# Kernel tuning notes

Hardware: AMD Instinct MI355X
Metric: run time of the kernel (lower is better)

The kernel has to match this reference:

```python
import jax, jax.numpy as jnp
from jax import lax
import numpy as np

B, C, Hf, Wf = 4, 256, 64, 64
COMP = max(C // 4, 16)  # 64
SCALE, K_UP, K_ENC = 2, 5, 3
EPS = 1e-5


def setup_inputs() -> dict:
    key = jax.random.key(0)
    ks = jax.random.split(key, 6)
    x = jax.random.normal(ks[0], (B, C, Hf, Wf), dtype=jnp.float32)
    w_comp = jax.random.normal(ks[1], (COMP, C), dtype=jnp.float32) * (1.0 / np.sqrt(C))
    bn_gamma = jnp.ones((COMP,), dtype=jnp.float32)
    bn_beta = jnp.zeros((COMP,), dtype=jnp.float32)
    bn_mean = jax.random.normal(ks[2], (COMP,), dtype=jnp.float32) * 0.1
    bn_var = jax.random.uniform(ks[3], (COMP,), dtype=jnp.float32, minval=0.5, maxval=1.5)
    w_enc = jax.random.normal(ks[4], (K_UP * K_UP * SCALE * SCALE, COMP, K_ENC, K_ENC), dtype=jnp.float32) * (1.0 / np.sqrt(COMP * K_ENC * K_ENC))
    return {"x": x, "w_comp": w_comp, "bn_gamma": bn_gamma, "bn_beta": bn_beta,
            "bn_mean": bn_mean, "bn_var": bn_var, "w_enc": w_enc}


def reference(x, w_comp, bn_gamma, bn_beta, bn_mean, bn_var, w_enc):
    b, c, h, w = x.shape
    s, k = SCALE, K_UP
    # 1x1 compression conv
    comp = jnp.einsum('bchw,oc->bohw', x, w_comp)
    # BatchNorm (eval-style, running stats) + SiLU
    inv = (bn_gamma / jnp.sqrt(bn_var + EPS))[:, None, None]
    bn = (comp - bn_mean[:, None, None]) * inv + bn_beta[:, None, None]
    act = bn * jax.nn.sigmoid(bn)
    # encoder conv -> per-pixel reassembly kernels, channels = k^2 * s^2 (k2 outer, s2 inner)
    mask = lax.conv_general_dilated(act, w_enc, (1, 1), ((1, 1), (1, 1)),
                                    dimension_numbers=('NCHW', 'OIHW', 'NCHW'))
    mask = mask.reshape(b, k * k, s * s, h, w)
    mask = jax.nn.softmax(mask, axis=1)  # softmax over k_up*k_up window
    # unfold: gather 5x5 neighborhoods (pad 2), k = dy*5+dx row-major like F.unfold
    pad = k // 2
    xp = jnp.pad(x, ((0, 0), (0, 0), (pad, pad), (pad, pad)))
    patches = jnp.stack([xp[:, :, dy:dy + h, dx:dx + w]
                         for dy in range(k) for dx in range(k)], axis=2)  # (b,c,k2,h,w)
    # content-aware weighted sum per sub-pixel position
    out = jnp.einsum('bksij,bckij->bcsij', mask, patches)  # (b,c,s2,h,w)
    # s2 -> (s0,s1); pixel (i*s+s0, j*s+s1)
    out = out.reshape(b, c, s, s, h, w).transpose(0, 1, 4, 2, 5, 3).reshape(b, c, h * s, w * s)
    return out
```

## Files before the change

### kernel.cpp

```cpp
#include <hip/hip_runtime.h>
#include <hip/hip_bf16.h>
#include <hip/hip_fp16.h>
#include <math.h>

#define B_ 4
#define C_ 256
#define H_ 64
#define W_ 64
#define COMP_ 64
#define K2_ 25
#define HW_ (H_*W_)
#define EPS_ 1e-5f
#define WTE_STRIDE 26

typedef float v2f __attribute__((ext_vector_type(2)));
#define FMA2(a, b, c) __builtin_elementwise_fma((a), (b), (c))

__global__ void k_transpose(const float* __restrict__ w_comp,
                            const float* __restrict__ w_enc,
                            float* __restrict__ wTc,
                            float* __restrict__ wTe) {
    int t = blockIdx.x * 256 + threadIdx.x;
    if (t < COMP_ * C_) {
        int o = t & 63;
        int c = t >> 6;
        wTc[t] = w_comp[o * C_ + c];
    } else {
        int t2 = t - COMP_ * C_;
        if (t2 < 100 * COMP_ * 9) {
            int k2 = t2 % 25;
            int r = t2 / 25;
            int s2 = r & 3; r >>= 2;
            int q = r % 9;
            int o = r / 9;
            wTe[((o * 9 + q) * 4 + s2) * WTE_STRIDE + k2] =
                w_enc[(((k2 * 4 + s2) * COMP_) + o) * 9 + q];
        }
    }
}

__global__ void __launch_bounds__(1024)
k_compress(const float* __restrict__ x, const float* __restrict__ wTc,
           const float* __restrict__ gamma, const float* __restrict__ beta,
           const float* __restrict__ mean, const float* __restrict__ var,
           float* __restrict__ act) {
    __shared__ v2f red[32 * 64];
    const int tx = threadIdx.x;
    const int ty = threadIdx.y;
    const int tz = threadIdx.z;
    const int ogu = __builtin_amdgcn_readfirstlane(ty);
    const int cgu = __builtin_amdgcn_readfirstlane(tz);
    const int b = blockIdx.y;
    const int p0 = blockIdx.x * 64;

    v2f acc2[4];
#pragma unroll
    for (int k = 0; k < 4; ++k) acc2[k] = (v2f){0.f, 0.f};

    const float* xb = x + (size_t)b * C_ * HW_ + p0 + tx;
#pragma unroll 8
    for (int cl = 0; cl < 128; ++cl) {
        int c = cgu * 128 + cl;
        float xv = xb[c * HW_];
        const v2f* w2 = (const v2f*)(wTc + c * COMP_ + ogu * 8);
        v2f xv2 = (v2f){xv, xv};
#pragma unroll
        for (int k = 0; k < 4; ++k)
            acc2[k] = FMA2(xv2, w2[k], acc2[k]);
    }

    if (tz == 1) {
#pragma unroll
        for (int k = 0; k < 4; ++k) red[(ty * 4 + k) * 64 + tx] = acc2[k];
    }
    __syncthreads();
    if (tz == 0) {
#pragma unroll
        for (int k = 0; k < 4; ++k) {
            v2f s = acc2[k] + red[(ty * 4 + k) * 64 + tx];
            int o0 = ty * 8 + 2 * k;
#pragma unroll
            for (int h = 0; h < 2; ++h) {
                int o = o0 + h;
                float sv = (h == 0) ? s.x : s.y;
                float iv = gamma[o] * rsqrtf(var[o] + EPS_);
                float bn = (sv - mean[o]) * iv + beta[o];
                float sg = 1.f / (1.f + __expf(-bn));
                act[((b * COMP_ + o) * HW_) + p0 + tx] = bn * sg;
            }
        }
    }
}

__global__ void __launch_bounds__(1024)
k_encoder(const float* __restrict__ act, const float* __restrict__ wTe,
          __half* __restrict__ maskT) {
    __shared__ float sact[13312];
    const int tx = threadIdx.x;
    const int ty = threadIdx.y;
    const int tz = threadIdx.z;
    const int tid = (tz * 4 + ty) * 64 + tx;
    const int i = blockIdx.x;
    const int b = blockIdx.y;
    const int s2u = __builtin_amdgcn_readfirstlane(ty);
    const int ogu = __builtin_amdgcn_readfirstlane(tz);

    const float* ab = act + (size_t)b * COMP_ * HW_;
    for (int t = tid; t < 3 * COMP_ * 66; t += 1024) {
        int col = t % 66;
        int r = t / 66;
        int o = r & 63;
        int row = r >> 6;
        int gi = i + row - 1;
        int gj = col - 1;
        float v = 0.f;
        if ((unsigned)gi < 64u && (unsigned)gj < 64u)
            v = ab[(o * H_ + gi) * W_ + gj];
        sact[t] = v;
    }
    __syncthreads();

    v2f acc2[13];
#pragma unroll
    for (int k = 0; k < 13; ++k) acc2[k] = (v2f){0.f, 0.f};

#pragma unroll 2
    for (int oi = 0; oi < 16; ++oi) {
        int o = ogu * 16 + oi;
#pragma unroll
        for (int q = 0; q < 9; ++q) {
            const int dy = q / 3, dx = q % 3;
            float a = sact[(dy * COMP_ + o) * 66 + tx + dx];
            const float* wb = wTe + ((o * 9 + q) * 4 + s2u) * WTE_STRIDE;
            const v2f* w2 = (const v2f*)wb;
            v2f a2 = (v2f){a, a};
#pragma unroll
            for (int k = 0; k < 12; ++k)
                acc2[k] = FMA2(a2, w2[k], acc2[k]);
            acc2[12].x = fmaf(wb[24], a, acc2[12].x);
        }
    }
    __syncthreads();

    v2f* bufA = (v2f*)sact;
    v2f* bufB = bufA + 3328;
    const int rix = ty * 64 + tx;
    if (tz == 1) {
#pragma unroll
        for (int k = 0; k < 13; ++k) bufA[k * 256 + rix] = acc2[k];
    } else if (tz == 2) {
#pragma unroll
        for (int k = 0; k < 13; ++k) bufB[k * 256 + rix] = acc2[k];
    }
    __syncthreads();
    if (tz == 0) {
#pragma unroll
        for (int k = 0; k < 13; ++k) acc2[k] += bufA[k * 256 + rix];
    } else if (tz == 3) {
#pragma unroll
        for (int k = 0; k < 13; ++k) acc2[k] += bufB[k * 256 + rix];
    }
    __syncthreads();
    if (tz == 3) {
#pragma unroll
        for (int k = 0; k < 13; ++k) bufA[k * 256 + rix] = acc2[k];
    }
    __syncthreads();
    float ex[K2_];
    if (tz == 0) {
#pragma unroll
        for (int k = 0; k < 13; ++k) acc2[k] += bufA[k * 256 + rix];

        float mx = acc2[12].x;
#pragma unroll
        for (int k = 0; k < 12; ++k) mx = fmaxf(mx, fmaxf(acc2[k].x, acc2[k].y));
        float sum = 0.f;
#pragma unroll
        for (int k = 0; k < 12; ++k) {
            ex[2 * k]     = __expf(acc2[k].x - mx);
            ex[2 * k + 1] = __expf(acc2[k].y - mx);
            sum += ex[2 * k] + ex[2 * k + 1];
        }
        ex[24] = __expf(acc2[12].x - mx);
        sum += ex[24];
        float rs = 1.f / sum;
#pragma unroll
        for (int k = 0; k < K2_; ++k) ex[k] *= rs;
    }
    __syncthreads();

    __half* st = (__half*)sact;
    if (tz == 0) {
#pragma unroll
        for (int k = 0; k < K2_; ++k)
            st[tx * 100 + k * 4 + ty] = __float2half(ex[k]);
    }
    __syncthreads();

    float4* dst = (float4*)(maskT + ((size_t)b * HW_ + i * 64) * 100);
    const float4* src = (const float4*)st;
    if (tid < 800) dst[tid] = src[tid];
}

__global__ void __launch_bounds__(256)
k_reassemble(const float* __restrict__ x, const __half* __restrict__ maskT,
             float* __restrict__ out) {
    __shared__ __align__(16) __half smask[64 * 100];
    __shared__ __align__(16) float sx[5 * 68 * 20];
    const int tx = threadIdx.x;
    const int ty = threadIdx.y;
    const int tid = ty * 64 + tx;
    const int i = blockIdx.x;
    const int cc = blockIdx.y;
    const int b = blockIdx.z;

    {
        const float4* src = (const float4*)(maskT + ((size_t)b * HW_ + i * 64) * 100);
        float4* dst = (float4*)smask;
#pragma unroll
        for (int t = 0; t < 4; ++t) {
            int e = tid + t * 256;
            if (e < 800) dst[e] = src[e];
        }
    }

    const float* xb = x + ((size_t)b * C_ + cc * 16 + ty * 4) * HW_;
#pragma unroll
    for (int r = 0; r < 5; ++r) {
        const int gi = i + r - 2;
        const bool rowok = ((unsigned)gi < 64u);
        {
            float4 v = {0.f, 0.f, 0.f, 0.f};
            int gj = tx - 2;
            if (rowok && gj >= 0) {
                const float* p = xb + gi * W_ + gj;
                v.x = p[0];
                v.y = p[HW_];
                v.z = p[2 * HW_];
                v.w = p[3 * HW_];
            }
            *(float4*)&sx[(r * 68 + tx) * 20 + ty * 4] = v;
        }
        if (tid < 16) {
            int q = tid >> 2;
            int col = 64 + (tid & 3);
            int gj = col - 2;
            float4 v = {0.f, 0.f, 0.f, 0.f};
            if (rowok && gj < 64) {
                const float* p = x + ((size_t)b * C_ + cc * 16 + q * 4) * HW_ + gi * W_ + gj;
                v.x = p[0];
                v.y = p[HW_];
                v.z = p[2 * HW_];
                v.w = p[3 * HW_];
            }
            *(float4*)&sx[(r * 68 + col) * 20 + q * 4] = v;
        }
    }
    __syncthreads();

    v2f a01[4], a23[4];
#pragma unroll
    for (int cl = 0; cl < 4; ++cl) { a01[cl] = (v2f){0.f, 0.f}; a23[cl] = (v2f){0.f, 0.f}; }

    float4 xq = *(const float4*)&sx[(0 * 68 + tx + 0) * 20 + ty * 4];
    __half2 h01 = *(const __half2*)&smask[tx * 100 + 0];
    __half2 h23 = *(const __half2*)&smask[tx * 100 + 2];

#pragma unroll
    for (int k2 = 0; k2 < K2_; ++k2) {
        float4 xq_c = xq;
        __half2 h01_c = h01, h23_c = h23;
        if (k2 < K2_ - 1) {
            const int kn = k2 + 1;
            const int dy = kn / 5, dx = kn % 5;
            xq  = *(const float4*)&sx[(dy * 68 + tx + dx) * 20 + ty * 4];
            h01 = *(const __half2*)&smask[tx * 100 + kn * 4];
            h23 = *(const __half2*)&smask[tx * 100 + kn * 4 + 2];
        }
        float2 f01 = __half22float2(h01_c);
        float2 f23 = __half22float2(h23_c);
        v2f m01 = (v2f){f01.x, f01.y};
        v2f m23 = (v2f){f23.x, f23.y};
        float xc[4] = {xq_c.x, xq_c.y, xq_c.z, xq_c.w};
#pragma unroll
        for (int cl = 0; cl < 4; ++cl) {
            v2f xv2 = (v2f){xc[cl], xc[cl]};
            a01[cl] = FMA2(xv2, m01, a01[cl]);
            a23[cl] = FMA2(xv2, m23, a23[cl]);
        }
    }

#pragma unroll
    for (int cl = 0; cl < 4; ++cl) {
        int c = cc * 16 + ty * 4 + cl;
        float* op = out + (((size_t)(b * C_ + c) * 128 + 2 * i) * 128) + 2 * tx;
        *(float2*)op         = float2{a01[cl].x, a01[cl].y};
        *(float2*)(op + 128) = float2{a23[cl].x, a23[cl].y};
    }
}

extern "C" void kernel_launch(void* const* d_in, const int* in_sizes, int n_in,
                              void* d_out, int out_size, void* d_ws, size_t ws_size,
                              hipStream_t stream) {
    const float* x       = (const float*)d_in[0];
    const float* w_comp  = (const float*)d_in[1];
    const float* bn_g    = (const float*)d_in[2];
    const float* bn_b    = (const float*)d_in[3];
    const float* bn_m    = (const float*)d_in[4];
    const float* bn_v    = (const float*)d_in[5];
    const float* w_enc   = (const float*)d_in[6];
    float* out = (float*)d_out;

    float* ws    = (float*)d_ws;
    float* wTc   = ws;
    float* wTe   = ws + 16384;
    float* act   = ws + 16384 + 59904;
    __half* maskT = (__half*)(act + (size_t)B_ * COMP_ * HW_);

    k_transpose<<<289, 256, 0, stream>>>(w_comp, w_enc, wTc, wTe);
    k_compress<<<dim3(64, B_), dim3(64, 8, 2), 0, stream>>>(x, wTc, bn_g, bn_b, bn_m, bn_v, act);
    k_encoder<<<dim3(64, B_), dim3(64, 4, 4), 0, stream>>>(act, wTe, maskT);
    k_reassemble<<<dim3(64, 16, B_), dim3(64, 4), 0, stream>>>(x, maskT, out);
}
```

Baseline: 169.0 us.

## Stage compress input via LDS float4 loads, swizzle reassemble blocks, batch global loads

k_compress now loads its 256x64 x tile into LDS with float4 loads using 512 threads, and drops the two-way channel split and its reduction step. k_reassemble flattens its grid to 1D and applies an XCD-aware block swizzle so neighbouring rows share L2. It also issues all mask and x halo loads into registers before writing them to LDS, which exposes more memory-level parallelism. The trade-offs are fewer threads in the compress kernel, higher register pressure in reassemble, and a 68KB LDS footprint for compress that limits occupancy.

```diff
diff --git a/kernel.cpp b/kernel.cpp
--- a/kernel.cpp
+++ b/kernel.cpp
@@ -39,29 +39,37 @@
     }
 }
 
-__global__ void __launch_bounds__(1024)
+__global__ void __launch_bounds__(512)
 k_compress(const float* __restrict__ x, const float* __restrict__ wTc,
            const float* __restrict__ gamma, const float* __restrict__ beta,
            const float* __restrict__ mean, const float* __restrict__ var,
            float* __restrict__ act) {
-    __shared__ v2f red[32 * 64];
+    __shared__ float sx[256 * 68];
     const int tx = threadIdx.x;
     const int ty = threadIdx.y;
-    const int tz = threadIdx.z;
+    const int tid = ty * 64 + tx;
     const int ogu = __builtin_amdgcn_readfirstlane(ty);
-    const int cgu = __builtin_amdgcn_readfirstlane(tz);
     const int b = blockIdx.y;
     const int p0 = blockIdx.x * 64;
 
+    const float* xb = x + (size_t)b * C_ * HW_ + p0;
+#pragma unroll
+    for (int l = 0; l < 8; ++l) {
+        int e = tid + l * 512;
+        int c = e >> 4;
+        int p4 = (e & 15) << 2;
+        float4 v4 = *(const float4*)(xb + (size_t)c * HW_ + p4);
+        *(float4*)&sx[c * 68 + p4] = v4;
+    }
+    __syncthreads();
+
     v2f acc2[4];
 #pragma unroll
     for (int k = 0; k < 4; ++k) acc2[k] = (v2f){0.f, 0.f};
 
-    const float* xb = x + (size_t)b * C_ * HW_ + p0 + tx;
 #pragma unroll 8
-    for (int cl = 0; cl < 128; ++cl) {
-        int c = cgu * 128 + cl;
-        float xv = xb[c * HW_];
+    for (int c = 0; c < 256; ++c) {
+        float xv = sx[c * 68 + tx];
         const v2f* w2 = (const v2f*)(wTc + c * COMP_ + ogu * 8);
         v2f xv2 = (v2f){xv, xv};
 #pragma unroll
@@ -69,25 +77,17 @@
             acc2[k] = FMA2(xv2, w2[k], acc2[k]);
     }
 
-    if (tz == 1) {
-#pragma unroll
-        for (int k = 0; k < 4; ++k) red[(ty * 4 + k) * 64 + tx] = acc2[k];
-    }
-    __syncthreads();
-    if (tz == 0) {
-#pragma unroll
-        for (int k = 0; k < 4; ++k) {
-            v2f s = acc2[k] + red[(ty * 4 + k) * 64 + tx];
-            int o0 = ty * 8 + 2 * k;
-#pragma unroll
-            for (int h = 0; h < 2; ++h) {
-                int o = o0 + h;
-                float sv = (h == 0) ? s.x : s.y;
-                float iv = gamma[o] * rsqrtf(var[o] + EPS_);
-                float bn = (sv - mean[o]) * iv + beta[o];
-                float sg = 1.f / (1.f + __expf(-bn));
-                act[((b * COMP_ + o) * HW_) + p0 + tx] = bn * sg;
-            }
+#pragma unroll
+    for (int k = 0; k < 4; ++k) {
+        int o0 = ty * 8 + 2 * k;
+#pragma unroll
+        for (int h = 0; h < 2; ++h) {
+            int o = o0 + h;
+            float sv = (h == 0) ? acc2[k].x : acc2[k].y;
+            float iv = gamma[o] * rsqrtf(var[o] + EPS_);
+            float bn = (sv - mean[o]) * iv + beta[o];
+            float sg = 1.f / (1.f + __expf(-bn));
+            act[((b * COMP_ + o) * HW_) + p0 + tx] = bn * sg;
         }
     }
 }
@@ -210,50 +210,59 @@
     const int tx = threadIdx.x;
     const int ty = threadIdx.y;
     const int tid = ty * 64 + tx;
-    const int i = blockIdx.x;
-    const int cc = blockIdx.y;
-    const int b = blockIdx.z;
+
+    const int bid = blockIdx.x;
+    const int wg  = ((bid & 7) << 9) | (bid >> 3);
+    const int cc = wg & 15;
+    const int i  = (wg >> 4) & 63;
+    const int b  = wg >> 10;
+
+    const float4* msrc = (const float4*)(maskT + ((size_t)b * HW_ + i * 64) * 100);
+    float4 vm[4];
+#pragma unroll
+    for (int t = 0; t < 4; ++t) {
+        int e = tid + t * 256;
+        vm[t] = (e < 800) ? msrc[e] : make_float4(0.f, 0.f, 0.f, 0.f);
+    }
+
+    float4 vx[6];
+#pragma unroll
+    for (int l = 0; l < 6; ++l) {
+        int e = tid + l * 256;
+        int q = e / 340;
+        int rem = e - q * 340;
+        int r = rem / 68;
+        int col = rem - r * 68;
+        int gi = i + r - 2;
+        int gj = col - 2;
+        float4 v = make_float4(0.f, 0.f, 0.f, 0.f);
+        if (e < 1360 && (unsigned)gi < 64u && (unsigned)gj < 64u) {
+            const float* p = x + ((size_t)b * C_ + cc * 16 + q * 4) * HW_ + gi * W_ + gj;
+            v.x = p[0];
+            v.y = p[HW_];
+            v.z = p[2 * HW_];
+            v.w = p[3 * HW_];
+        }
+        vx[l] = v;
+    }
 
     {
-        const float4* src = (const float4*)(maskT + ((size_t)b * HW_ + i * 64) * 100);
-        float4* dst = (float4*)smask;
+        float4* mdst = (float4*)smask;
 #pragma unroll
         for (int t = 0; t < 4; ++t) {
             int e = tid + t * 256;
-            if (e < 800) dst[e] = src[e];
-        }
-    }
-
-    const float* xb = x + ((size_t)b * C_ + cc * 16 + ty * 4) * HW_;
-#pragma unroll
-    for (int r = 0; r < 5; ++r) {
-        const int gi = i + r - 2;
-        const bool rowok = ((unsigned)gi < 64u);
-        {
-            float4 v = {0.f, 0.f, 0.f, 0.f};
-            int gj = tx - 2;
-            if (rowok && gj >= 0) {
-                const float* p = xb + gi * W_ + gj;
-                v.x = p[0];
-                v.y = p[HW_];
-                v.z = p[2 * HW_];
-                v.w = p[3 * HW_];
-            }
-            *(float4*)&sx[(r * 68 + tx) * 20 + ty * 4] = v;
-        }
-        if (tid < 16) {
-            int q = tid >> 2;
-            int col = 64 + (tid & 3);
-            int gj = col - 2;
-            float4 v = {0.f, 0.f, 0.f, 0.f};
-            if (rowok && gj < 64) {
-                const float* p = x + ((size_t)b * C_ + cc * 16 + q * 4) * HW_ + gi * W_ + gj;
-                v.x = p[0];
-                v.y = p[HW_];
-                v.z = p[2 * HW_];
-                v.w = p[3 * HW_];
-            }
-            *(float4*)&sx[(r * 68 + col) * 20 + q * 4] = v;
+            if (e < 800) mdst[e] = vm[t];
+        }
+    }
+#pragma unroll
+    for (int l = 0; l < 6; ++l) {
+        int e = tid + l * 256;
+        if (e < 1360) {
+            int q = e / 340;
+            int rem = e - q * 340;
+            int r = rem / 68;
+            int col = rem - r * 68;
+            *(float4*)&sx[(r * 68 + col) * 20 + q * 4] = vx[l];
         }
     }
     __syncthreads();
@@ -318,7 +327,7 @@
     __half* maskT = (__half*)(act + (size_t)B_ * COMP_ * HW_);
 
     k_transpose<<<289, 256, 0, stream>>>(w_comp, w_enc, wTc, wTe);
-    k_compress<<<dim3(64, B_), dim3(64, 8, 2), 0, stream>>>(x, wTc, bn_g, bn_b, bn_m, bn_v, act);
+    k_compress<<<dim3(64, B_), dim3(64, 8), 0, stream>>>(x, wTc, bn_g, bn_b, bn_m, bn_v, act);
     k_encoder<<<dim3(64, B_), dim3(64, 4, 4), 0, stream>>>(act, wTe, maskT);
-    k_reassemble<<<dim3(64, 16, B_), dim3(64, 4), 0, stream>>>(x, maskT, out);
-}
+    k_reassemble<<<4096, dim3(64, 4), 0, stream>>>(x, maskT, out);
+}
```

Measured after the change: 163.4 us. -3.3%, faster.

## Move encoder conv to fp16 MFMA with packed weights and channel-last fp16 activations

Applied to the files above, without the earlier changes.

The 3x3 encoder convolution becomes an implicit GEMM on MFMA 16x16x32 f16 instructions. Weights are prepacked into per-lane fragments, and activations are stored as fp16 in pixel-major layout. The compress kernel now stages x through shared memory and drops the split-channel reduction. The reassemble kernel uses a swizzled 1D grid so blocks that share mask and x data run close together. Using fp16 for activations and weights adds rounding error in the mask logits before the softmax.

```diff
diff --git a/kernel.cpp b/kernel.cpp
--- a/kernel.cpp
+++ b/kernel.cpp
@@ -11,15 +11,16 @@
 #define K2_ 25
 #define HW_ (H_*W_)
 #define EPS_ 1e-5f
-#define WTE_STRIDE 26
 
 typedef float v2f __attribute__((ext_vector_type(2)));
+typedef float f32x4 __attribute__((ext_vector_type(4)));
+typedef _Float16 half8 __attribute__((ext_vector_type(8)));
 #define FMA2(a, b, c) __builtin_elementwise_fma((a), (b), (c))
 
 __global__ void k_transpose(const float* __restrict__ w_comp,
                             const float* __restrict__ w_enc,
                             float* __restrict__ wTc,
-                            float* __restrict__ wTe) {
+                            __half* __restrict__ Apack) {
     int t = blockIdx.x * 256 + threadIdx.x;
     if (t < COMP_ * C_) {
         int o = t & 63;
@@ -27,41 +28,56 @@
         wTc[t] = w_comp[o * C_ + c];
     } else {
         int t2 = t - COMP_ * C_;
-        if (t2 < 100 * COMP_ * 9) {
-            int k2 = t2 % 25;
-            int r = t2 / 25;
-            int s2 = r & 3; r >>= 2;
-            int q = r % 9;
-            int o = r / 9;
-            wTe[((o * 9 + q) * 4 + s2) * WTE_STRIDE + k2] =
-                w_enc[(((k2 * 4 + s2) * COMP_) + o) * 9 + q];
-        }
-    }
-}
-
-__global__ void __launch_bounds__(1024)
+        if (t2 < 8 * 18 * 64) {
+            int lane = t2 & 63;
+            int ks   = (t2 >> 6) % 18;
+            int MT   = t2 / (64 * 18);
+            int m    = MT * 16 + (lane & 15);
+            __half vals[8];
+#pragma unroll
+            for (int e = 0; e < 8; ++e) {
+                int k = ks * 32 + (lane >> 4) * 8 + e;
+                int q = k >> 6;
+                int c = k & 63;
+                float wv = (m < 100) ? w_enc[(m * COMP_ + c) * 9 + q] : 0.f;
+                vals[e] = __float2half(wv);
+            }
+            *(float4*)&Apack[(size_t)t2 * 8] = *(float4*)vals;
+        }
+    }
+}
+
+__global__ void __launch_bounds__(512)
 k_compress(const float* __restrict__ x, const float* __restrict__ wTc,
            const float* __restrict__ gamma, const float* __restrict__ beta,
            const float* __restrict__ mean, const float* __restrict__ var,
-           float* __restrict__ act) {
-    __shared__ v2f red[32 * 64];
+           __half* __restrict__ act16) {
+    __shared__ float sx[256 * 68];
     const int tx = threadIdx.x;
     const int ty = threadIdx.y;
-    const int tz = threadIdx.z;
+    const int tid = ty * 64 + tx;
     const int ogu = __builtin_amdgcn_readfirstlane(ty);
-    const int cgu = __builtin_amdgcn_readfirstlane(tz);
-    const int b = blockIdx.y;
+    const int bb = blockIdx.y;
     const int p0 = blockIdx.x * 64;
 
+    const float* xb = x + (size_t)bb * C_ * HW_ + p0;
+#pragma unroll
+    for (int l = 0; l < 8; ++l) {
+        int e = tid + l * 512;
+        int c = e >> 4;
+        int p4 = (e & 15) << 2;
+        float4 v4 = *(const float4*)(xb + (size_t)c * HW_ + p4);
+        *(float4*)&sx[c * 68 + p4] = v4;
+    }
+    __syncthreads();
+
     v2f acc2[4];
 #pragma unroll
     for (int k = 0; k < 4; ++k) acc2[k] = (v2f){0.f, 0.f};
 
-    const float* xb = x + (size_t)b * C_ * HW_ + p0 + tx;
 #pragma unroll 8
-    for (int cl = 0; cl < 128; ++cl) {
-        int c = cgu * 128 + cl;
-        float xv = xb[c * HW_];
+    for (int c = 0; c < 256; ++c) {
+        float xv = sx[c * 68 + tx];
         const v2f* w2 = (const v2f*)(wTc + c * COMP_ + ogu * 8);
         v2f xv2 = (v2f){xv, xv};
 #pragma unroll
@@ -69,137 +85,114 @@
             acc2[k] = FMA2(xv2, w2[k], acc2[k]);
     }
 
-    if (tz == 1) {
-#pragma unroll
-        for (int k = 0; k < 4; ++k) red[(ty * 4 + k) * 64 + tx] = acc2[k];
-    }
-    __syncthreads();
-    if (tz == 0) {
-#pragma unroll
-        for (int k = 0; k < 4; ++k) {
-            v2f s = acc2[k] + red[(ty * 4 + k) * 64 + tx];
-            int o0 = ty * 8 + 2 * k;
-#pragma unroll
-            for (int h = 0; h < 2; ++h) {
-                int o = o0 + h;
-                float sv = (h == 0) ? s.x : s.y;
-                float iv = gamma[o] * rsqrtf(var[o] + EPS_);
-                float bn = (sv - mean[o]) * iv + beta[o];
-                float sg = 1.f / (1.f + __expf(-bn));
-                act[((b * COMP_ + o) * HW_) + p0 + tx] = bn * sg;
-            }
-        }
-    }
-}
-
-__global__ void __launch_bounds__(1024)
-k_encoder(const float* __restrict__ act, const float* __restrict__ wTe,
+    __half h8[8];
+#pragma unroll
+    for (int k = 0; k < 4; ++k) {
+#pragma unroll
+        for (int h = 0; h < 2; ++h) {
+            int o = ty * 8 + 2 * k + h;
+            float sv = (h == 0) ? acc2[k].x : acc2[k].y;
+            float iv = gamma[o] * rsqrtf(var[o] + EPS_);
+            float bn = (sv - mean[o]) * iv + beta[o];
+            float sg = 1.f / (1.f + __expf(-bn));
+            h8[2 * k + h] = __float2half(bn * sg);
+        }
+    }
+    __syncthreads();
+    __half* sxh = (__half*)sx;
+    *(float2*)&sxh[tx * 68 + ty * 8]     = *(float2*)&h8[0];
+    *(float2*)&sxh[tx * 68 + ty * 8 + 4] = *(float2*)&h8[4];
+    __syncthreads();
+
+    {
+        int px = tid >> 3, c8 = tid & 7;
+        float2 alo = *(float2*)&sxh[px * 68 + c8 * 8];
+        float2 ahi = *(float2*)&sxh[px * 68 + c8 * 8 + 4];
+        float4 v = make_float4(alo.x, alo.y, ahi.x, ahi.y);
+        __half* ao = act16 + ((size_t)bb * HW_ + p0 + px) * COMP_ + c8 * 8;
+        *(float4*)ao = v;
+    }
+}
+
+__global__ void __launch_bounds__(512)
+k_encoder(const __half* __restrict__ act16, const __half* __restrict__ Apack,
           __half* __restrict__ maskT) {
-    __shared__ float sact[13312];
-    const int tx = threadIdx.x;
-    const int ty = threadIdx.y;
-    const int tz = threadIdx.z;
-    const int tid = (tz * 4 + ty) * 64 + tx;
-    const int i = blockIdx.x;
-    const int b = blockIdx.y;
-    const int s2u = __builtin_amdgcn_readfirstlane(ty);
-    const int ogu = __builtin_amdgcn_readfirstlane(tz);
-
-    const float* ab = act + (size_t)b * COMP_ * HW_;
-    for (int t = tid; t < 3 * COMP_ * 66; t += 1024) {
-        int col = t % 66;
-        int r = t / 66;
-        int o = r & 63;
-        int row = r >> 6;
-        int gi = i + row - 1;
-        int gj = col - 1;
-        float v = 0.f;
-        if ((unsigned)gi < 64u && (unsigned)gj < 64u)
-            v = ab[(o * H_ + gi) * W_ + gj];
-        sact[t] = v;
-    }
-    __syncthreads();
-
-    v2f acc2[13];
-#pragma unroll
-    for (int k = 0; k < 13; ++k) acc2[k] = (v2f){0.f, 0.f};
-
-#pragma unroll 2
-    for (int oi = 0; oi < 16; ++oi) {
-        int o = ogu * 16 + oi;
-#pragma unroll
-        for (int q = 0; q < 9; ++q) {
-            const int dy = q / 3, dx = q % 3;
-            float a = sact[(dy * COMP_ + o) * 66 + tx + dx];
-            const float* wb = wTe + ((o * 9 + q) * 4 + s2u) * WTE_STRIDE;
-            const v2f* w2 = (const v2f*)wb;
-            v2f a2 = (v2f){a, a};
-#pragma unroll
-            for (int k = 0; k < 12; ++k)
-                acc2[k] = FMA2(a2, w2[k], acc2[k]);
-            acc2[12].x = fmaf(wb[24], a, acc2[12].x);
-        }
-    }
-    __syncthreads();
-
-    v2f* bufA = (v2f*)sact;
-    v2f* bufB = bufA + 3328;
-    const int rix = ty * 64 + tx;
-    if (tz == 1) {
-#pragma unroll
-        for (int k = 0; k < 13; ++k) bufA[k * 256 + rix] = acc2[k];
-    } else if (tz == 2) {
-#pragma unroll
-        for (int k = 0; k < 13; ++k) bufB[k * 256 + rix] = acc2[k];
-    }
-    __syncthreads();
-    if (tz == 0) {
-#pragma unroll
-        for (int k = 0; k < 13; ++k) acc2[k] += bufA[k * 256 + rix];
-    } else if (tz == 3) {
-#pragma unroll
-        for (int k = 0; k < 13; ++k) acc2[k] += bufB[k * 256 + rix];
-    }
-    __syncthreads();
-    if (tz == 3) {
-#pragma unroll
-        for (int k = 0; k < 13; ++k) bufA[k * 256 + rix] = acc2[k];
-    }
-    __syncthreads();
-    float ex[K2_];
-    if (tz == 0) {
-#pragma unroll
-        for (int k = 0; k < 13; ++k) acc2[k] += bufA[k * 256 + rix];
-
-        float mx = acc2[12].x;
-#pragma unroll
-        for (int k = 0; k < 12; ++k) mx = fmaxf(mx, fmaxf(acc2[k].x, acc2[k].y));
+    __shared__ __align__(16) __half sact[3 * 66 * 80];
+    __shared__ float cbuf[64 * 129];
+    __shared__ __align__(16) __half st[64 * 100];
+    const int tid = threadIdx.x;
+    const int i = blockIdx.x, b = blockIdx.y;
+    const int lane = tid & 63, w = tid >> 6;
+
+    const __half* ab = act16 + (size_t)b * HW_ * COMP_;
+    {
+        int col = tid >> 3, c8 = tid & 7;
+#pragma unroll
+        for (int r = 0; r < 3; ++r) {
+            int gi = i + r - 1;
+            float4 v = make_float4(0.f, 0.f, 0.f, 0.f);
+            if ((unsigned)gi < 64u)
+                v = *(const float4*)(ab + ((size_t)gi * 64 + col) * COMP_ + c8 * 8);
+            *(float4*)((char*)sact + (size_t)(r * 66 + col + 1) * 160 + c8 * 16) = v;
+        }
+    }
+    if (tid < 60) {
+        int pl = tid / 10, sl = tid % 10;
+        int r = pl >> 1, col = (pl & 1) * 65;
+        *(float4*)((char*)sact + (size_t)(r * 66 + col) * 160 + sl * 16) =
+            make_float4(0.f, 0.f, 0.f, 0.f);
+    }
+    __syncthreads();
+
+    const int j0 = (w & 3) * 16;
+    const int MT0 = (w >> 2) * 4;
+    const int p = lane & 15, g = lane >> 4;
+    f32x4 acc[4];
+#pragma unroll
+    for (int mt = 0; mt < 4; ++mt) acc[mt] = (f32x4){0.f, 0.f, 0.f, 0.f};
+    const half8* Ap = (const half8*)Apack;
+#pragma unroll
+    for (int ks = 0; ks < 18; ++ks) {
+        const int q = ks >> 1, ky = q / 3, kx = q % 3;
+        half8 bf = *(const half8*)((const char*)sact +
+                       (size_t)(ky * 66 + j0 + p + kx) * 160 +
+                       ((ks & 1) * 32 + g * 8) * 2);
+#pragma unroll
+        for (int mt = 0; mt < 4; ++mt) {
+            half8 af = Ap[((size_t)(MT0 + mt) * 18 + ks) * 64 + lane];
+            acc[mt] = __builtin_amdgcn_mfma_f32_16x16x32_f16(af, bf, acc[mt], 0, 0, 0);
+        }
+    }
+
+#pragma unroll
+    for (int mt = 0; mt < 4; ++mt)
+#pragma unroll
+        for (int r4 = 0; r4 < 4; ++r4)
+            cbuf[(j0 + p) * 129 + (MT0 + mt) * 16 + g * 4 + r4] = acc[mt][r4];
+    __syncthreads();
+
+    if (tid < 256) {
+        int px = tid & 63, s2 = tid >> 6;
+        float v[K2_];
+        float mx = -1e30f;
+#pragma unroll
+        for (int k2 = 0; k2 < K2_; ++k2) {
+            v[k2] = cbuf[px * 129 + k2 * 4 + s2];
+            mx = fmaxf(mx, v[k2]);
+        }
         float sum = 0.f;
 #pragma unroll
-        for (int k = 0; k < 12; ++k) {
-            ex[2 * k]     = __expf(acc2[k].x - mx);
-            ex[2 * k + 1] = __expf(acc2[k].y - mx);
-            sum += ex[2 * k] + ex[2 * k + 1];
-        }
-        ex[24] = __expf(acc2[12].x - mx);
-        sum += ex[24];
+        for (int k2 = 0; k2 < K2_; ++k2) { v[k2] = __expf(v[k2] - mx); sum += v[k2]; }
         float rs = 1.f / sum;
 #pragma unroll
-        for (int k = 0; k < K2_; ++k) ex[k] *= rs;
-    }
-    __syncthreads();
-
-    __half* st = (__half*)sact;
-    if (tz == 0) {
-#pragma unroll
-        for (int k = 0; k < K2_; ++k)
-            st[tx * 100 + k * 4 + ty] = __float2half(ex[k]);
+        for (int k2 = 0; k2 < K2_; ++k2)
+            st[px * 100 + k2 * 4 + s2] = __float2half(v[k2] * rs);
     }
     __syncthreads();
 
     float4* dst = (float4*)(maskT + ((size_t)b * HW_ + i * 64) * 100);
     const float4* src = (const float4*)st;
-    if (tid < 800) dst[tid] = src[tid];
+    for (int e = tid; e < 800; e += 512) dst[e] = src[e];
 }
 
 __global__ void __launch_bounds__(256)
@@ -210,9 +203,12 @@
     const int tx = threadIdx.x;
     const int ty = threadIdx.y;
     const int tid = ty * 64 + tx;
-    const int i = blockIdx.x;
-    const int cc = blockIdx.y;
-    const int b = blockIdx.z;
+
+    const int bid = blockIdx.x;
+    const int id  = ((bid & 7) << 9) | (bid >> 3);
+    const int cc = id & 15;
+    const int i  = (id >> 4) & 63;
+    const int b  = id >> 10;
 
     {
         const float4* src = (const float4*)(maskT + ((size_t)b * HW_ + i * 64) * 100);
@@ -311,14 +307,14 @@
     const float* w_enc   = (const float*)d_in[6];
     float* out = (float*)d_out;
 
-    float* ws    = (float*)d_ws;
-    float* wTc   = ws;
-    float* wTe   = ws + 16384;
-    float* act   = ws + 16384 + 59904;
-    __half* maskT = (__half*)(act + (size_t)B_ * COMP_ * HW_);
-
-    k_transpose<<<289, 256, 0, stream>>>(w_comp, w_enc, wTc, wTe);
-    k_compress<<<dim3(64, B_), dim3(64, 8, 2), 0, stream>>>(x, wTc, bn_g, bn_b, bn_m, bn_v, act);
-    k_encoder<<<dim3(64, B_), dim3(64, 4, 4), 0, stream>>>(act, wTe, maskT);
-    k_reassemble<<<dim3(64, 16, B_), dim3(64, 4), 0, stream>>>(x, maskT, out);
-}
+    float* ws     = (float*)d_ws;
+    float* wTc    = ws;
+    __half* Apack = (__half*)(ws + 16384);
+    __half* act16 = (__half*)(ws + 53248);
+    __half* maskT = (__half*)(ws + 577536);
+
+    k_transpose<<<100, 256, 0, stream>>>(w_comp, w_enc, wTc, Apack);
+    k_compress<<<dim3(64, B_), dim3(64, 8), 0, stream>>>(x, wTc, bn_g, bn_b, bn_m, bn_v, act16);
+    k_encoder<<<dim3(64, B_), 512, 0, stream>>>(act16, Apack, maskT);
+    k_reassemble<<<4096, dim3(64, 4), 0, stream>>>(x, maskT, out);
+}
```

After: 147.2 us. 12.9% less time.
